# Optimization experiments

Measured on AMD Instinct MI355X. Metric: run time of the kernel, lower is better.

Reference implementation:

```python
import jax, jax.numpy as jnp
import numpy as np

N_GRAPHS = 512
NODES_PER_G = 200
EDGES_PER_G = 6400
N = N_GRAPHS * NODES_PER_G        # 102400 nodes
E = N_GRAPHS * EDGES_PER_G        # 3276800 edges
HID = 128
NCLS = 10


def _linear_params(key, fan_in, fan_out):
    # torch nn.Linear default init: U(-1/sqrt(fan_in), 1/sqrt(fan_in))
    s = 1.0 / np.sqrt(fan_in)
    kw, kb = jax.random.split(key)
    W = jax.random.uniform(kw, (fan_in, fan_out), minval=-s, maxval=s, dtype=jnp.float32)
    b = jax.random.uniform(kb, (fan_out,), minval=-s, maxval=s, dtype=jnp.float32)
    return W, b


def setup_inputs() -> dict:
    key = jax.random.key(0)
    ks = jax.random.split(key, 10)
    # edges are confined within each graph (DGL batched graph structure)
    g_off = (jnp.arange(E, dtype=jnp.int32) // EDGES_PER_G) * NODES_PER_G
    src = (g_off + jax.random.randint(ks[0], (E,), 0, NODES_PER_G)).astype(jnp.int32)
    dst = (g_off + jax.random.randint(ks[1], (E,), 0, NODES_PER_G)).astype(jnp.int32)
    W1, b1 = _linear_params(ks[2], 1, HID)
    W2, b2 = _linear_params(ks[3], HID, HID)
    Wa, ba = _linear_params(ks[4], HID, 512)
    Wb, bb = _linear_params(ks[5], 512, 1024)
    Wc, bc = _linear_params(ks[6], 1024, 1024)
    Wd, bd = _linear_params(ks[7], 1024, 512)
    We, be = _linear_params(ks[8], 512, NCLS)
    return dict(src=src, dst=dst, W1=W1, b1=b1, W2=W2, b2=b2,
                Wa=Wa, ba=ba, Wb=Wb, bb=bb, Wc=Wc, bc=bc,
                Wd=Wd, bd=bd, We=We, be=be)


def reference(src, dst, W1, b1, W2, b2, Wa, ba, Wb, bb, Wc, bc, Wd, bd, We, be):
    seg = jax.ops.segment_sum
    ones = jnp.ones((E,), jnp.float32)
    in_deg = seg(ones, dst, num_segments=N)    # [N]
    out_deg = seg(ones, src, num_segments=N)   # [N]
    # DGL GraphConv norm='both': degrees clamped to min 1
    inv_out = (1.0 / jnp.sqrt(jnp.maximum(out_deg, 1.0)))[:, None]
    inv_in = (1.0 / jnp.sqrt(jnp.maximum(in_deg, 1.0)))[:, None]

    def gconv(h, W, b):
        h = (h @ W) * inv_out                    # src-side normalize (weight applied first; same math)
        h = seg(h[src], dst, num_segments=N)     # gather + scatter-add aggregation
        return h * inv_in + b                    # dst-side normalize + bias

    h = in_deg[:, None]                          # input node features = in-degrees, [N,1]
    h = jax.nn.relu(gconv(h, W1, b1))
    h = jax.nn.relu(gconv(h, W2, b2))

    gid = jnp.arange(N, dtype=jnp.int32) // NODES_PER_G
    hg = seg(h, gid, num_segments=N_GRAPHS) / float(NODES_PER_G)  # mean readout, [G,HID]

    x = jax.nn.relu(hg @ Wa + ba)
    x = jax.nn.relu(x @ Wb + bb)
    x = jax.nn.relu(x @ Wc + bc)
    x = jax.nn.relu(x @ Wd + bd)
    return jax.nn.softmax(x @ We + be, axis=-1)  # nn.Softmax over class dim
```

## Files before the change

### kernel.cpp

```cpp
#include <hip/hip_runtime.h>
#include <stdint.h>

typedef unsigned short u16;
typedef unsigned int   u32;

#define NG   512
#define NPG  200
#define EPG  6400
#define NN   (NG*NPG)
#define NE_  (NG*EPG)
#define HID  128
#define HS   232
#define ZP   136

__device__ __forceinline__ float bf2f(u16 b){ u32 u = ((u32)b) << 16; return __builtin_bit_cast(float, u); }
__device__ __forceinline__ u16 f2bf(float f){
    u32 u = __builtin_bit_cast(u32, f);
    u = (u + 0x7FFFu + ((u >> 16) & 1u)) >> 16;
    return (u16)u;
}

typedef __attribute__((ext_vector_type(8))) short bf16x8;
typedef __attribute__((ext_vector_type(4))) float f32x4;

enum : int { cW1=0, cb1=128, cb2=256, cba=384, cbb=896, cbc=1920, cbd=2944, cWe=3456, cbe=8576, cEND=8586 };
enum : int { T_Wa=0, T_Wb=65536, T_Wc=589824, T_Wd=1638400, T_END=2162688 };

struct PrepIn { const void* p[14]; };

__global__ __launch_bounds__(256) void k_prep2(PrepIn in, float* __restrict__ canon,
                                               u16* __restrict__ W2T, u16* __restrict__ WTa)
{
    __shared__ u16 tile[64][72];
    __shared__ int sflag;
    const int tid = threadIdx.x;
    if (tid < 64){
        const u16* wb = (const u16*)in.p[0];
        u16 a = wb[tid], b = wb[64 + tid];
        unsigned long long m1 = __ballot((int)((a >> 7) & 0xFF) >= 0x7F);
        unsigned long long m2 = __ballot((int)((b >> 7) & 0xFF) >= 0x7F);
        if (tid == 0) sflag = (__popcll(m1) + __popcll(m2) > 4) ? 1 : 0;
    }
    __syncthreads();
    const int f = sflag;
    const int bid = blockIdx.x;

    if (bid < 532){
        const void* s; u16* dst; int K, N, t, lgn;
        if      (bid < 4)  { t = bid;       s = in.p[2];  dst = W2T;        K = 128;  N = 128;  lgn = 1; }
        else if (bid < 20) { t = bid - 4;   s = in.p[4];  dst = WTa + T_Wa; K = 128;  N = 512;  lgn = 3; }
        else if (bid < 148){ t = bid - 20;  s = in.p[6];  dst = WTa + T_Wb; K = 512;  N = 1024; lgn = 4; }
        else if (bid < 404){ t = bid - 148; s = in.p[8];  dst = WTa + T_Wc; K = 1024; N = 1024; lgn = 4; }
        else               { t = bid - 404; s = in.p[10]; dst = WTa + T_Wd; K = 1024; N = 512;  lgn = 3; }
        const int k0 = (t >> lgn) * 64, n0 = (t & ((1 << lgn) - 1)) * 64;
        #pragma unroll
        for (int i = 0; i < 16; i++){
            int idx = i*256 + tid;
            int kk = idx >> 6, nn = idx & 63;
            int si = (k0 + kk)*N + n0 + nn;
            tile[nn][kk] = f ? f2bf(((const float*)s)[si]) : ((const u16*)s)[si];
        }
        __syncthreads();
        #pragma unroll
        for (int i = 0; i < 16; i++){
            int idx = i*256 + tid;
            int nn = idx >> 6, kk = idx & 63;
            dst[(size_t)(n0 + nn)*K + k0 + kk] = tile[nn][kk];
        }
    } else {
        int i = (bid - 532)*256 + tid;
        if (i < cEND){
            const void* s; int off;
            if      (i < 128) { s = in.p[0];  off = i; }
            else if (i < 256) { s = in.p[1];  off = i - 128; }
            else if (i < 384) { s = in.p[3];  off = i - 256; }
            else if (i < 896) { s = in.p[5];  off = i - 384; }
            else if (i < 1920){ s = in.p[7];  off = i - 896; }
            else if (i < 2944){ s = in.p[9];  off = i - 1920; }
            else if (i < 3456){ s = in.p[11]; off = i - 2944; }
            else if (i < 8576){ s = in.p[12]; off = i - 3456; }
            else              { s = in.p[13]; off = i - 8576; }
            canon[i] = f ? ((const float*)s)[off] : bf2f(((const u16*)s)[off]);
        }
    }
}

__global__ __launch_bounds__(512) void k_mega(
    const int* __restrict__ src, const int* __restrict__ dst,
    const float* __restrict__ W1, const float* __restrict__ b1,
    const float* __restrict__ b2, const u16* __restrict__ W2T,
    float* __restrict__ hg)
{
    __shared__ u32 pkE[EPG];
    __shared__ __align__(16) u16 h1s[HID*HS];
    __shared__ __align__(16) u16 Aq[64*HS];
    __shared__ __align__(16) u16 Zq[64*ZP];
    __shared__ int degIn[NPG], degOut[NPG];
    __shared__ float sVal[NPG], sAgg[NPG], iiL[NPG], ioL[NPG], tL[NPG];
    __shared__ float w1L[HID], b1L[HID], b2L[HID], poolL[HID];

    const int g = blockIdx.x, tid = threadIdx.x;
    u32* aq32 = (u32*)Aq;

    if (tid < NPG){ degIn[tid] = 0; degOut[tid] = 0; sAgg[tid] = 0.f; }
    if (tid < HID){ w1L[tid] = W1[tid]; b1L[tid] = b1[tid]; b2L[tid] = b2[tid]; poolL[tid] = 0.f; }
    __syncthreads();

    const int ebase = g * EPG;
    #pragma unroll
    for (int i = 0; i < (EPG + 511)/512; i++){
        int e = i*512 + tid;
        if (e < EPG){
            int s = src[ebase + e] - g*NPG;
            int d = dst[ebase + e] - g*NPG;
            pkE[e] = (u32)s | ((u32)d << 16);
            atomicAdd(&degOut[s], 1);
            atomicAdd(&degIn[d], 1);
        }
    }
    __syncthreads();

    if (tid < NPG){
        float ii = rsqrtf(fmaxf((float)degIn[tid], 1.f));
        float io = rsqrtf(fmaxf((float)degOut[tid], 1.f));
        iiL[tid] = ii; ioL[tid] = io;
        sVal[tid] = (float)degIn[tid] * io;
    }
    __syncthreads();

    #pragma unroll
    for (int i = 0; i < (EPG + 511)/512; i++){
        int e = i*512 + tid;
        if (e < EPG){
            u32 u = pkE[e];
            atomicAdd(&sAgg[u >> 16], sVal[u & 0xFFFF]);
        }
    }
    __syncthreads();
    if (tid < NPG) tL[tid] = sAgg[tid] * iiL[tid];
    __syncthreads();

    #pragma unroll 4
    for (int i = 0; i < HID*HS/512; i++){
        int idx = i*512 + tid;
        int c = idx / HS, v = idx - c*HS;
        u16 o = 0;
        if (v < NPG)
            o = f2bf(fmaxf(fmaf(tL[v], w1L[c], b1L[c]), 0.f) * ioL[v]);
        h1s[idx] = o;
    }
    __syncthreads();

    const int w = tid >> 6, lane = tid & 63;
    const int lr = lane & 15, quad = lane >> 4;
    const f32x4 fz = {0.f, 0.f, 0.f, 0.f};

    for (int q = 0; q < 4; q++){
        uint4* a4 = (uint4*)Aq;
        for (int i = tid; i < 64*HS/8; i += 512) a4[i] = make_uint4(0,0,0,0);
        __syncthreads();
        #pragma unroll
        for (int i = 0; i < (EPG + 511)/512; i++){
            int e = i*512 + tid;
            if (e < EPG){
                u32 u = pkE[e];
                int s = u & 0xFFFF, d = u >> 16;
                int qe = (d * 41) >> 11;
                if (qe == q){
                    int idx = (d - q*50)*HS + s;
                    atomicAdd(&aq32[idx >> 1], 1u << (16*(idx & 1)));
                }
            }
        }
        __syncthreads();
        for (int i = tid; i < 64*HS/2; i += 512){
            u32 wv = aq32[i];
            if (wv)
                aq32[i] = (u32)f2bf((float)(wv & 0xFFFFu)) | ((u32)f2bf((float)(wv >> 16)) << 16);
        }
        __syncthreads();

        const int wm = w >> 1, wn = w & 1;
        f32x4 acc[2][2];
        #pragma unroll
        for (int mi = 0; mi < 2; mi++)
            #pragma unroll
            for (int nt = 0; nt < 2; nt++) acc[mi][nt] = fz;
        for (int ks = 0; ks < 7; ks++){
            bf16x8 af[2], bf[2];
            #pragma unroll
            for (int mi = 0; mi < 2; mi++)
                af[mi] = *(const bf16x8*)&h1s[(wm*32 + mi*16 + lr)*HS + ks*32 + quad*8];
            #pragma unroll
            for (int nt = 0; nt < 2; nt++)
                bf[nt] = *(const bf16x8*)&Aq[(wn*32 + nt*16 + lr)*HS + ks*32 + quad*8];
            #pragma unroll
            for (int mi = 0; mi < 2; mi++)
                #pragma unroll
                for (int nt = 0; nt < 2; nt++)
                    acc[mi][nt] = __builtin_amdgcn_mfma_f32_16x16x32_bf16(
                        af[mi], bf[nt], acc[mi][nt], 0, 0, 0);
        }
        #pragma unroll
        for (int mi = 0; mi < 2; mi++)
            #pragma unroll
            for (int nt = 0; nt < 2; nt++){
                int vq = wn*32 + nt*16 + lr;
                int c0 = wm*32 + mi*16 + quad*4;
                u16 z0 = f2bf(acc[mi][nt][0]), z1 = f2bf(acc[mi][nt][1]);
                u16 z2 = f2bf(acc[mi][nt][2]), z3 = f2bf(acc[mi][nt][3]);
                uint2 pk = { (u32)z0 | ((u32)z1 << 16), (u32)z2 | ((u32)z3 << 16) };
                *(uint2*)&Zq[vq*ZP + c0] = pk;
            }
        __syncthreads();

        const int wm2 = w >> 2, wn2 = w & 3;
        f32x4 acc2[2][2];
        #pragma unroll
        for (int mi = 0; mi < 2; mi++)
            #pragma unroll
            for (int nt = 0; nt < 2; nt++) acc2[mi][nt] = fz;
        for (int ks = 0; ks < 4; ks++){
            bf16x8 za[2], wb[2];
            #pragma unroll
            for (int mi = 0; mi < 2; mi++)
                za[mi] = *(const bf16x8*)&Zq[(wm2*32 + mi*16 + lr)*ZP + ks*32 + quad*8];
            #pragma unroll
            for (int nt = 0; nt < 2; nt++)
                wb[nt] = *(const bf16x8*)&W2T[(size_t)(wn2*32 + nt*16 + lr)*HID + ks*32 + quad*8];
            #pragma unroll
            for (int mi = 0; mi < 2; mi++)
                #pragma unroll
                for (int nt = 0; nt < 2; nt++)
                    acc2[mi][nt] = __builtin_amdgcn_mfma_f32_16x16x32_bf16(
                        za[mi], wb[nt], acc2[mi][nt], 0, 0, 0);
        }
        #pragma unroll
        for (int mi = 0; mi < 2; mi++)
            #pragma unroll
            for (int nt = 0; nt < 2; nt++){
                int cout = wn2*32 + nt*16 + lr;
                float s = 0.f;
                #pragma unroll
                for (int r = 0; r < 4; r++){
                    int vq = wm2*32 + mi*16 + quad*4 + r;
                    if (vq < 50)
                        s += fmaxf(fmaf(acc2[mi][nt][r], iiL[q*50 + vq], b2L[cout]), 0.f);
                }
                atomicAdd(&poolL[cout], s);
            }
        __syncthreads();
    }

    if (tid < HID) hg[(size_t)g*HID + tid] = poolL[tid] * (1.f / NPG);
}

template<int K, bool AF32>
__global__ __launch_bounds__(512) void k_mlp5(
    const void* __restrict__ Ahi_, const u16* __restrict__ Alo,
    const u16* __restrict__ WT, const float* __restrict__ bias,
    u16* __restrict__ Ohi, u16* __restrict__ Olo, int Nc)
{
    constexpr int ITERS = K / 64;
    __shared__ __align__(16) float red[32][68];

    const int tid = threadIdx.x;
    const int w = tid >> 6, lane = tid & 63;
    const int kz = w >> 2, wm = (w >> 1) & 1, wn = w & 1;
    const int lr = lane & 15, quad = lane >> 4;
    const int row0 = blockIdx.x * 32, col0 = blockIdx.y * 64;
    const int m = row0 + wm*16 + lr;
    const int k0 = kz * (K/2);

    const float* Af = (const float*)Ahi_;
    const u16*   Ah = (const u16*)Ahi_;

    auto loadA = [&](int it, bf16x8& hi, bf16x8& lo){
        const int kk = k0 + it*32 + quad*8;
        if constexpr (AF32){
            float xs[8];
            *(float4*)&xs[0] = *(const float4*)&Af[(size_t)m*K + kk];
            *(float4*)&xs[4] = *(const float4*)&Af[(size_t)m*K + kk + 4];
            #pragma unroll
            for (int j = 0; j < 8; j++){
                u16 hh = f2bf(xs[j]);
                hi[j] = (short)hh;
                lo[j] = (short)f2bf(xs[j] - bf2f(hh));
            }
        } else {
            hi = *(const bf16x8*)&Ah[(size_t)m*K + kk];
            lo = *(const bf16x8*)&Alo[(size_t)m*K + kk];
        }
    };
    auto loadB = [&](int it, bf16x8* b){
        const int kk = k0 + it*32 + quad*8;
        #pragma unroll
        for (int nt = 0; nt < 2; nt++){
            int n = col0 + wn*32 + nt*16 + lr;
            b[nt] = *(const bf16x8*)&WT[(size_t)n*K + kk];
        }
    };

    const f32x4 fz = {0.f, 0.f, 0.f, 0.f};
    f32x4 acc[2] = {fz, fz};
    bf16x8 chi, clo, cb[2], nhi, nlo, nb[2];
    loadA(0, chi, clo); loadB(0, cb);
    #pragma unroll 2
    for (int it = 0; it < ITERS; it++){
        if (it + 1 < ITERS){ loadA(it+1, nhi, nlo); loadB(it+1, nb); }
        #pragma unroll
        for (int nt = 0; nt < 2; nt++){
            acc[nt] = __builtin_amdgcn_mfma_f32_16x16x32_bf16(chi, cb[nt], acc[nt], 0, 0, 0);
            acc[nt] = __builtin_amdgcn_mfma_f32_16x16x32_bf16(clo, cb[nt], acc[nt], 0, 0, 0);
        }
        chi = nhi; clo = nlo; cb[0] = nb[0]; cb[1] = nb[1];
    }

    if (kz == 1){
        #pragma unroll
        for (int nt = 0; nt < 2; nt++)
            #pragma unroll
            for (int r = 0; r < 4; r++)
                red[wm*16 + quad*4 + r][wn*32 + nt*16 + lr] = acc[nt][r];
    }
    __syncthreads();
    if (kz == 0){
        #pragma unroll
        for (int nt = 0; nt < 2; nt++)
            #pragma unroll
            for (int r = 0; r < 4; r++){
                int rr = wm*16 + quad*4 + r;
                int cc = wn*32 + nt*16 + lr;
                float v = acc[nt][r] + red[rr][cc] + bias[col0 + cc];
                v = fmaxf(v, 0.f);
                u16 hh = f2bf(v);
                size_t go = (size_t)(row0 + rr) * Nc + col0 + cc;
                Ohi[go] = hh;
                Olo[go] = f2bf(v - bf2f(hh));
            }
    }
}

__global__ __launch_bounds__(64) void k_head(
    const u16* __restrict__ Xhi, const u16* __restrict__ Xlo,
    const float* __restrict__ We, const float* __restrict__ be,
    void* __restrict__ out, const u16* __restrict__ w1bits)
{
    const int g = blockIdx.x, lane = threadIdx.x;
    u16 a = w1bits[lane], b = w1bits[64 + lane];
    unsigned long long m1 = __ballot((int)((a >> 7) & 0xFF) >= 0x7F);
    unsigned long long m2 = __ballot((int)((b >> 7) & 0xFF) >= 0x7F);
    const int f = (__popcll(m1) + __popcll(m2) > 4) ? 1 : 0;

    float part[10];
    #pragma unroll
    for (int c = 0; c < 10; c++) part[c] = 0.f;
    for (int k = lane; k < 512; k += 64){
        float x = bf2f(Xhi[(size_t)g*512 + k]) + bf2f(Xlo[(size_t)g*512 + k]);
        #pragma unroll
        for (int c = 0; c < 10; c++) part[c] = fmaf(x, We[k*10 + c], part[c]);
    }
    #pragma unroll
    for (int c = 0; c < 10; c++){
        float v = part[c];
        for (int off = 32; off > 0; off >>= 1) v += __shfl_down(v, off);
        part[c] = v;
    }
    if (lane == 0){
        #pragma unroll
        for (int c = 0; c < 10; c++) part[c] += be[c];
        float m = part[0];
        #pragma unroll
        for (int c = 1; c < 10; c++) m = fmaxf(m, part[c]);
        float e[10], s = 0.f;
        #pragma unroll
        for (int c = 0; c < 10; c++){ e[c] = __expf(part[c] - m); s += e[c]; }
        float inv = 1.f / s;
        #pragma unroll
        for (int c = 0; c < 10; c++){
            float p = e[c] * inv;
            if (f) ((float*)out)[g*10 + c] = p;
            else   ((u16*)out)[g*10 + c]  = f2bf(p);
        }
    }
}

extern "C" void kernel_launch(void* const* d_in, const int* in_sizes, int n_in,
                              void* d_out, int out_size, void* d_ws, size_t ws_size,
                              hipStream_t stream)
{
    const int* src = (const int*)d_in[0];
    const int* dst = (const int*)d_in[1];

    char* ws = (char*)d_ws;
    size_t o = 0;
    float* canon    = (float*)(ws + o); o += ((size_t)cEND * 4 + 15) & ~(size_t)15;
    u16*   W2T      = (u16*)  (ws + o); o += (size_t)HID * HID * 2;
    u16*   WTa      = (u16*)  (ws + o); o += ((size_t)T_END * 2 + 15) & ~(size_t)15;
    float* hg       = (float*)(ws + o); o += (size_t)NG * HID * 4;
    u16*   X1hi     = (u16*)  (ws + o); o += (size_t)NG * 512 * 2;
    u16*   X1lo     = (u16*)  (ws + o); o += (size_t)NG * 512 * 2;
    u16*   X2hi     = (u16*)  (ws + o); o += (size_t)NG * 1024 * 2;
    u16*   X2lo     = (u16*)  (ws + o); o += (size_t)NG * 1024 * 2;
    u16*   X3hi     = (u16*)  (ws + o); o += (size_t)NG * 1024 * 2;
    u16*   X3lo     = (u16*)  (ws + o); o += (size_t)NG * 1024 * 2;
    u16*   X4hi     = (u16*)  (ws + o); o += (size_t)NG * 512 * 2;
    u16*   X4lo     = (u16*)  (ws + o); o += (size_t)NG * 512 * 2;
    (void)ws_size; (void)in_sizes; (void)n_in; (void)out_size;

    PrepIn pin;
    for (int i = 0; i < 14; i++) pin.p[i] = d_in[2 + i];
    k_prep2<<<dim3(566), dim3(256), 0, stream>>>(pin, canon, W2T, WTa);

    const float *W1 = canon+cW1, *b1 = canon+cb1, *b2 = canon+cb2;
    const float *ba = canon+cba, *bb = canon+cbb, *bc = canon+cbc, *bd = canon+cbd;
    const float *We = canon+cWe, *be = canon+cbe;

    k_mega<<<dim3(NG), dim3(512), 0, stream>>>(src, dst, W1, b1, b2, W2T, hg);

    k_mlp5<128,  true ><<<dim3(16, 8),  dim3(512), 0, stream>>>(hg,   nullptr, WTa + T_Wa, ba, X1hi, X1lo, 512);
    k_mlp5<512,  false><<<dim3(16, 16), dim3(512), 0, stream>>>(X1hi, X1lo,    WTa + T_Wb, bb, X2hi, X2lo, 1024);
    k_mlp5<1024, false><<<dim3(16, 16), dim3(512), 0, stream>>>(X2hi, X2lo,    WTa + T_Wc, bc, X3hi, X3lo, 1024);
    k_mlp5<1024, false><<<dim3(16, 8),  dim3(512), 0, stream>>>(X3hi, X3lo,    WTa + T_Wd, bd, X4hi, X4lo, 512);

    k_head<<<dim3(NG), dim3(64), 0, stream>>>(X4hi, X4lo, We, be, d_out, (const u16*)d_in[2]);
}
```

Measured before the change: 255.7 us.

## Shrink LDS in graph mega-kernel and deepen MLP GEMM prefetch

The per-graph kernel now keeps the packed edge list in registers instead of LDS. It builds the first-layer features in two 64-channel halves rebuilt for each quarter, and reuses the adjacency buffer for Z. This cuts shared-memory use so more blocks fit per CU (launch_bounds 512,4), and W2T fragments are hoisted into registers outside the quarter loop. In exchange, h1 is recomputed four times, register pressure rises, and the dense GEMM kernel gets a 3-stage register prefetch with full unroll.

```diff
diff --git a/kernel.cpp b/kernel.cpp
--- a/kernel.cpp
+++ b/kernel.cpp
@@ -85,37 +85,42 @@
     }
 }
 
-__global__ __launch_bounds__(512) void k_mega(
+__global__ __launch_bounds__(512, 4) void k_mega(
     const int* __restrict__ src, const int* __restrict__ dst,
     const float* __restrict__ W1, const float* __restrict__ b1,
     const float* __restrict__ b2, const u16* __restrict__ W2T,
     float* __restrict__ hg)
 {
-    __shared__ u32 pkE[EPG];
-    __shared__ __align__(16) u16 h1s[HID*HS];
-    __shared__ __align__(16) u16 Aq[64*HS];
-    __shared__ __align__(16) u16 Zq[64*ZP];
+    __shared__ __align__(16) u16 h1sH[64*HS];
+    __shared__ __align__(16) u16 AqZ[64*HS];
     __shared__ int degIn[NPG], degOut[NPG];
     __shared__ float sVal[NPG], sAgg[NPG], iiL[NPG], ioL[NPG], tL[NPG];
     __shared__ float w1L[HID], b1L[HID], b2L[HID], poolL[HID];
 
     const int g = blockIdx.x, tid = threadIdx.x;
-    u32* aq32 = (u32*)Aq;
-
-    if (tid < NPG){ degIn[tid] = 0; degOut[tid] = 0; sAgg[tid] = 0.f; }
-    if (tid < HID){ w1L[tid] = W1[tid]; b1L[tid] = b1[tid]; b2L[tid] = b2[tid]; poolL[tid] = 0.f; }
-    __syncthreads();
-
+    u32* aq32 = (u32*)AqZ;
+
+    u32 epk[13];
     const int ebase = g * EPG;
     #pragma unroll
-    for (int i = 0; i < (EPG + 511)/512; i++){
+    for (int i = 0; i < 13; i++){
         int e = i*512 + tid;
         if (e < EPG){
             int s = src[ebase + e] - g*NPG;
             int d = dst[ebase + e] - g*NPG;
-            pkE[e] = (u32)s | ((u32)d << 16);
-            atomicAdd(&degOut[s], 1);
-            atomicAdd(&degIn[d], 1);
+            epk[i] = (u32)s | ((u32)d << 16);
+        } else epk[i] = 0xFFFFFFFFu;
+    }
+
+    if (tid < NPG){ degIn[tid] = 0; degOut[tid] = 0; sAgg[tid] = 0.f; }
+    if (tid < HID){ w1L[tid] = W1[tid]; b1L[tid] = b1[tid]; b2L[tid] = b2[tid]; poolL[tid] = 0.f; }
+    __syncthreads();
+
+    #pragma unroll
+    for (int i = 0; i < 13; i++){
+        if (epk[i] != 0xFFFFFFFFu){
+            atomicAdd(&degOut[epk[i] & 0xFFFF], 1);
+            atomicAdd(&degIn[epk[i] >> 16], 1);
         }
     }
     __syncthreads();
@@ -129,45 +134,39 @@
     __syncthreads();
 
     #pragma unroll
-    for (int i = 0; i < (EPG + 511)/512; i++){
-        int e = i*512 + tid;
-        if (e < EPG){
-            u32 u = pkE[e];
-            atomicAdd(&sAgg[u >> 16], sVal[u & 0xFFFF]);
-        }
+    for (int i = 0; i < 13; i++){
+        if (epk[i] != 0xFFFFFFFFu)
+            atomicAdd(&sAgg[epk[i] >> 16], sVal[epk[i] & 0xFFFF]);
     }
     __syncthreads();
     if (tid < NPG) tL[tid] = sAgg[tid] * iiL[tid];
-    __syncthreads();
-
-    #pragma unroll 4
-    for (int i = 0; i < HID*HS/512; i++){
-        int idx = i*512 + tid;
-        int c = idx / HS, v = idx - c*HS;
-        u16 o = 0;
-        if (v < NPG)
-            o = f2bf(fmaxf(fmaf(tL[v], w1L[c], b1L[c]), 0.f) * ioL[v]);
-        h1s[idx] = o;
-    }
-    __syncthreads();
 
     const int w = tid >> 6, lane = tid & 63;
     const int lr = lane & 15, quad = lane >> 4;
+    const int wm = w >> 1, wn = w & 1;
+    const int wm2 = w >> 2, wn2 = w & 3;
     const f32x4 fz = {0.f, 0.f, 0.f, 0.f};
 
+    bf16x8 wb[4][2];
+    #pragma unroll
+    for (int ks = 0; ks < 4; ks++)
+        #pragma unroll
+        for (int nt = 0; nt < 2; nt++)
+            wb[ks][nt] = *(const bf16x8*)&W2T[(size_t)(wn2*32 + nt*16 + lr)*HID + ks*32 + quad*8];
+    __syncthreads();
+
     for (int q = 0; q < 4; q++){
-        uint4* a4 = (uint4*)Aq;
+        uint4* a4 = (uint4*)AqZ;
         for (int i = tid; i < 64*HS/8; i += 512) a4[i] = make_uint4(0,0,0,0);
         __syncthreads();
         #pragma unroll
-        for (int i = 0; i < (EPG + 511)/512; i++){
-            int e = i*512 + tid;
-            if (e < EPG){
-                u32 u = pkE[e];
-                int s = u & 0xFFFF, d = u >> 16;
+        for (int i = 0; i < 13; i++){
+            u32 u = epk[i];
+            if (u != 0xFFFFFFFFu){
+                int d = u >> 16;
                 int qe = (d * 41) >> 11;
                 if (qe == q){
-                    int idx = (d - q*50)*HS + s;
+                    int idx = (d - q*50)*HS + (u & 0xFFFF);
                     atomicAdd(&aq32[idx >> 1], 1u << (16*(idx & 1)));
                 }
             }
@@ -180,61 +179,64 @@
         }
         __syncthreads();
 
-        const int wm = w >> 1, wn = w & 1;
-        f32x4 acc[2][2];
-        #pragma unroll
-        for (int mi = 0; mi < 2; mi++)
-            #pragma unroll
-            for (int nt = 0; nt < 2; nt++) acc[mi][nt] = fz;
-        for (int ks = 0; ks < 7; ks++){
-            bf16x8 af[2], bf[2];
-            #pragma unroll
-            for (int mi = 0; mi < 2; mi++)
-                af[mi] = *(const bf16x8*)&h1s[(wm*32 + mi*16 + lr)*HS + ks*32 + quad*8];
-            #pragma unroll
-            for (int nt = 0; nt < 2; nt++)
-                bf[nt] = *(const bf16x8*)&Aq[(wn*32 + nt*16 + lr)*HS + ks*32 + quad*8];
-            #pragma unroll
-            for (int mi = 0; mi < 2; mi++)
+        f32x4 accZ[2][2];
+        #pragma unroll
+        for (int h = 0; h < 2; h++){
+            #pragma unroll 4
+            for (int i = 0; i < 64*HS/512; i++){
+                int idx = i*512 + tid;
+                int cl = idx / HS, v = idx - cl*HS;
+                int c = h*64 + cl;
+                u16 o = 0;
+                if (v < NPG)
+                    o = f2bf(fmaxf(fmaf(tL[v], w1L[c], b1L[c]), 0.f) * ioL[v]);
+                h1sH[idx] = o;
+            }
+            __syncthreads();
+            accZ[h][0] = fz; accZ[h][1] = fz;
+            for (int ks = 0; ks < 7; ks++){
+                bf16x8 af = *(const bf16x8*)&h1sH[(wm*16 + lr)*HS + ks*32 + quad*8];
                 #pragma unroll
-                for (int nt = 0; nt < 2; nt++)
-                    acc[mi][nt] = __builtin_amdgcn_mfma_f32_16x16x32_bf16(
-                        af[mi], bf[nt], acc[mi][nt], 0, 0, 0);
-        }
-        #pragma unroll
-        for (int mi = 0; mi < 2; mi++)
+                for (int nt = 0; nt < 2; nt++){
+                    bf16x8 bfr = *(const bf16x8*)&AqZ[(wn*32 + nt*16 + lr)*HS + ks*32 + quad*8];
+                    accZ[h][nt] = __builtin_amdgcn_mfma_f32_16x16x32_bf16(af, bfr, accZ[h][nt], 0, 0, 0);
+                }
+            }
+            __syncthreads();
+        }
+
+        u16* Zq = AqZ;
+        #pragma unroll
+        for (int h = 0; h < 2; h++)
             #pragma unroll
             for (int nt = 0; nt < 2; nt++){
                 int vq = wn*32 + nt*16 + lr;
-                int c0 = wm*32 + mi*16 + quad*4;
-                u16 z0 = f2bf(acc[mi][nt][0]), z1 = f2bf(acc[mi][nt][1]);
-                u16 z2 = f2bf(acc[mi][nt][2]), z3 = f2bf(acc[mi][nt][3]);
+                int c0 = h*64 + wm*16 + quad*4;
+                u16 z0 = f2bf(accZ[h][nt][0]), z1 = f2bf(accZ[h][nt][1]);
+                u16 z2 = f2bf(accZ[h][nt][2]), z3 = f2bf(accZ[h][nt][3]);
                 uint2 pk = { (u32)z0 | ((u32)z1 << 16), (u32)z2 | ((u32)z3 << 16) };
                 *(uint2*)&Zq[vq*ZP + c0] = pk;
             }
         __syncthreads();
 
-        const int wm2 = w >> 2, wn2 = w & 3;
         f32x4 acc2[2][2];
         #pragma unroll
         for (int mi = 0; mi < 2; mi++)
             #pragma unroll
             for (int nt = 0; nt < 2; nt++) acc2[mi][nt] = fz;
         for (int ks = 0; ks < 4; ks++){
-            bf16x8 za[2], wb[2];
+            bf16x8 za[2];
             #pragma unroll
             for (int mi = 0; mi < 2; mi++)
                 za[mi] = *(const bf16x8*)&Zq[(wm2*32 + mi*16 + lr)*ZP + ks*32 + quad*8];
-            #pragma unroll
-            for (int nt = 0; nt < 2; nt++)
-                wb[nt] = *(const bf16x8*)&W2T[(size_t)(wn2*32 + nt*16 + lr)*HID + ks*32 + quad*8];
             #pragma unroll
             for (int mi = 0; mi < 2; mi++)
                 #pragma unroll
                 for (int nt = 0; nt < 2; nt++)
                     acc2[mi][nt] = __builtin_amdgcn_mfma_f32_16x16x32_bf16(
-                        za[mi], wb[nt], acc2[mi][nt], 0, 0, 0);
-        }
+                        za[mi], wb[ks][nt], acc2[mi][nt], 0, 0, 0);
+        }
+
         #pragma unroll
         for (int mi = 0; mi < 2; mi++)
             #pragma unroll
@@ -303,17 +305,19 @@
 
     const f32x4 fz = {0.f, 0.f, 0.f, 0.f};
     f32x4 acc[2] = {fz, fz};
-    bf16x8 chi, clo, cb[2], nhi, nlo, nb[2];
-    loadA(0, chi, clo); loadB(0, cb);
-    #pragma unroll 2
+    bf16x8 hi[3], lo[3], bb[3][2];
+    loadA(0, hi[0], lo[0]); loadB(0, bb[0]);
+    if (ITERS > 1){ loadA(1, hi[1], lo[1]); loadB(1, bb[1]); }
+    #pragma unroll
     for (int it = 0; it < ITERS; it++){
-        if (it + 1 < ITERS){ loadA(it+1, nhi, nlo); loadB(it+1, nb); }
+        const int sl = it % 3;
+        const int pf = (it + 2) % 3;
+        if (it + 2 < ITERS){ loadA(it+2, hi[pf], lo[pf]); loadB(it+2, bb[pf]); }
         #pragma unroll
         for (int nt = 0; nt < 2; nt++){
-            acc[nt] = __builtin_amdgcn_mfma_f32_16x16x32_bf16(chi, cb[nt], acc[nt], 0, 0, 0);
-            acc[nt] = __builtin_amdgcn_mfma_f32_16x16x32_bf16(clo, cb[nt], acc[nt], 0, 0, 0);
-        }
-        chi = nhi; clo = nlo; cb[0] = nb[0]; cb[1] = nb[1];
+            acc[nt] = __builtin_amdgcn_mfma_f32_16x16x32_bf16(hi[sl], bb[sl][nt], acc[nt], 0, 0, 0);
+            acc[nt] = __builtin_amdgcn_mfma_f32_16x16x32_bf16(lo[sl], bb[sl][nt], acc[nt], 0, 0, 0);
+        }
     }
 
     if (kz == 1){
```

New measurement: 261.4 us. +2.2%, slower.

## Split graph megakernel into layer-1 and per-quarter kernels; narrow MLP tiles

Applied to the files above, without the earlier changes.

The per-graph megakernel is split into two kernels. k_l1 computes degrees and the layer-1 features, writes h1 to global memory, and buckets edges into per-quarter lists. k_quarter then processes each graph quarter in its own block, with atomically accumulated pooling into hg, which k_prep2 now zeroes. This gives 4x more blocks for the layer-2 aggregation and GEMMs, and each block scans only its own quarter's edges instead of all edges four times. In exchange it adds global round-trips for h1sT and the edge buffers, uses a fixed QCAP that silently drops edges if a quarter overflows, and halves the MLP column tile with a 3-stage register prefetch to double the grid.

```diff
diff --git a/kernel.cpp b/kernel.cpp
--- a/kernel.cpp
+++ b/kernel.cpp
@@ -10,8 +10,10 @@
 #define NN   (NG*NPG)
 #define NE_  (NG*EPG)
 #define HID  128
-#define HS   232
+#define KP   224
+#define AQS  232
 #define ZP   136
+#define QCAP 2048
 
 __device__ __forceinline__ float bf2f(u16 b){ u32 u = ((u32)b) << 16; return __builtin_bit_cast(float, u); }
 __device__ __forceinline__ u16 f2bf(float f){
@@ -29,7 +31,8 @@
 struct PrepIn { const void* p[14]; };
 
 __global__ __launch_bounds__(256) void k_prep2(PrepIn in, float* __restrict__ canon,
-                                               u16* __restrict__ W2T, u16* __restrict__ WTa)
+                                               u16* __restrict__ W2T, u16* __restrict__ WTa,
+                                               float* __restrict__ hg)
 {
     __shared__ u16 tile[64][72];
     __shared__ int sflag;
@@ -44,6 +47,11 @@
     __syncthreads();
     const int f = sflag;
     const int bid = blockIdx.x;
+
+    if (tid < 116){
+        int j = bid*116 + tid;
+        if (j < NG*HID) hg[j] = 0.f;
+    }
 
     if (bid < 532){
         const void* s; u16* dst; int K, N, t, lgn;
@@ -85,38 +93,39 @@
     }
 }
 
-__global__ __launch_bounds__(512) void k_mega(
+__global__ __launch_bounds__(256) void k_l1(
     const int* __restrict__ src, const int* __restrict__ dst,
     const float* __restrict__ W1, const float* __restrict__ b1,
-    const float* __restrict__ b2, const u16* __restrict__ W2T,
-    float* __restrict__ hg)
-{
-    __shared__ u32 pkE[EPG];
-    __shared__ __align__(16) u16 h1s[HID*HS];
-    __shared__ __align__(16) u16 Aq[64*HS];
-    __shared__ __align__(16) u16 Zq[64*ZP];
+    float* __restrict__ invInG, u16* __restrict__ h1sT,
+    u32* __restrict__ edgeBuf, int* __restrict__ cntQ)
+{
+    __shared__ u16 srcL[EPG];
+    __shared__ u16 dstL[EPG];
     __shared__ int degIn[NPG], degOut[NPG];
-    __shared__ float sVal[NPG], sAgg[NPG], iiL[NPG], ioL[NPG], tL[NPG];
-    __shared__ float w1L[HID], b1L[HID], b2L[HID], poolL[HID];
+    __shared__ int qcur[4];
+    __shared__ float sAgg4[4][NPG];
+    __shared__ float sValL[NPG], iiL[NPG], ioL[NPG], tL[NPG];
+    __shared__ float w1L[HID], b1L[HID];
 
     const int g = blockIdx.x, tid = threadIdx.x;
-    u32* aq32 = (u32*)Aq;
-
-    if (tid < NPG){ degIn[tid] = 0; degOut[tid] = 0; sAgg[tid] = 0.f; }
-    if (tid < HID){ w1L[tid] = W1[tid]; b1L[tid] = b1[tid]; b2L[tid] = b2[tid]; poolL[tid] = 0.f; }
+
+    if (tid < NPG){
+        degIn[tid] = 0; degOut[tid] = 0;
+        sAgg4[0][tid] = 0.f; sAgg4[1][tid] = 0.f; sAgg4[2][tid] = 0.f; sAgg4[3][tid] = 0.f;
+    }
+    if (tid < HID){ w1L[tid] = W1[tid]; b1L[tid] = b1[tid]; }
+    if (tid < 4) qcur[tid] = 0;
     __syncthreads();
 
     const int ebase = g * EPG;
     #pragma unroll
-    for (int i = 0; i < (EPG + 511)/512; i++){
-        int e = i*512 + tid;
-        if (e < EPG){
-            int s = src[ebase + e] - g*NPG;
-            int d = dst[ebase + e] - g*NPG;
-            pkE[e] = (u32)s | ((u32)d << 16);
-            atomicAdd(&degOut[s], 1);
-            atomicAdd(&degIn[d], 1);
-        }
+    for (int i = 0; i < EPG/256; i++){
+        int e = i*256 + tid;
+        int s = src[ebase + e] - g*NPG;
+        int d = dst[ebase + e] - g*NPG;
+        srcL[e] = (u16)s; dstL[e] = (u16)d;
+        atomicAdd(&degOut[s], 1);
+        atomicAdd(&degIn[d], 1);
     }
     __syncthreads();
 
@@ -124,152 +133,206 @@
         float ii = rsqrtf(fmaxf((float)degIn[tid], 1.f));
         float io = rsqrtf(fmaxf((float)degOut[tid], 1.f));
         iiL[tid] = ii; ioL[tid] = io;
-        sVal[tid] = (float)degIn[tid] * io;
-    }
-    __syncthreads();
-
-    #pragma unroll
-    for (int i = 0; i < (EPG + 511)/512; i++){
-        int e = i*512 + tid;
-        if (e < EPG){
-            u32 u = pkE[e];
-            atomicAdd(&sAgg[u >> 16], sVal[u & 0xFFFF]);
-        }
-    }
-    __syncthreads();
-    if (tid < NPG) tL[tid] = sAgg[tid] * iiL[tid];
-    __syncthreads();
-
+        sValL[tid] = (float)degIn[tid] * io;
+        invInG[g*NPG + tid] = ii;
+    }
+    __syncthreads();
+
+    const int rep = tid & 3;
+    #pragma unroll
+    for (int i = 0; i < EPG/256; i++){
+        int e = i*256 + tid;
+        int s = srcL[e], d = dstL[e];
+        atomicAdd(&sAgg4[rep][d], sValL[s]);
+        int q = (d * 41) >> 11;
+        int pos = atomicAdd(&qcur[q], 1);
+        if (pos < QCAP)
+            edgeBuf[((size_t)(g*4 + q))*QCAP + pos] = (u32)s | ((u32)(d - q*50) << 16);
+    }
+    __syncthreads();
+
+    if (tid < 4) cntQ[g*4 + tid] = (qcur[tid] < QCAP) ? qcur[tid] : QCAP;
+    if (tid < NPG)
+        tL[tid] = (sAgg4[0][tid] + sAgg4[1][tid] + sAgg4[2][tid] + sAgg4[3][tid]) * iiL[tid];
+    __syncthreads();
+
+    const size_t base = (size_t)g * HID * KP;
     #pragma unroll 4
-    for (int i = 0; i < HID*HS/512; i++){
-        int idx = i*512 + tid;
-        int c = idx / HS, v = idx - c*HS;
+    for (int i = 0; i < HID*KP/256; i++){
+        int idx = i*256 + tid;
+        int c = idx / KP, v = idx - c*KP;
         u16 o = 0;
         if (v < NPG)
             o = f2bf(fmaxf(fmaf(tL[v], w1L[c], b1L[c]), 0.f) * ioL[v]);
-        h1s[idx] = o;
+        h1sT[base + idx] = o;
+    }
+}
+
+__global__ __launch_bounds__(256, 5) void k_quarter(
+    const u32* __restrict__ edgeBuf, const int* __restrict__ cntQ,
+    const u16* __restrict__ h1sT, const u16* __restrict__ W2T,
+    const float* __restrict__ invInG, const float* __restrict__ b2,
+    float* __restrict__ hg)
+{
+    __shared__ __align__(16) u16 Aq[64*AQS];
+    __shared__ float invInL[64];
+    __shared__ float b2L[HID];
+    __shared__ float poolL[HID];
+
+    const int bid = blockIdx.x, tid = threadIdx.x;
+    const int xcd = bid & 7, slot = bid >> 3;
+    const int g = (slot >> 2) * 8 + xcd;
+    const int q = slot & 3;
+    u32* aq32 = (u32*)Aq;
+
+    if (tid < HID){ b2L[tid] = b2[tid]; poolL[tid] = 0.f; }
+    if (tid < 64) invInL[tid] = (tid < 50) ? invInG[g*NPG + q*50 + tid] : 0.f;
+
+    uint4* a4 = (uint4*)Aq;
+    #pragma unroll
+    for (int i = 0; i < 8; i++){
+        int idx = i*256 + tid;
+        if (idx < 64*AQS/8) a4[idx] = make_uint4(0,0,0,0);
+    }
+    __syncthreads();
+
+    const int cnt = cntQ[g*4 + q];
+    const u32* eb = edgeBuf + (size_t)(g*4 + q) * QCAP;
+    for (int i = tid; i < cnt; i += 256){
+        u32 e = eb[i];
+        int idx = (int)(e >> 16) * AQS + (int)(e & 0xFFFF);
+        atomicAdd(&aq32[idx >> 1], 1u << (16*(idx & 1)));
+    }
+    __syncthreads();
+
+    for (int i = tid; i < 64*AQS/2; i += 256){
+        u32 wv = aq32[i];
+        if (wv)
+            aq32[i] = (u32)f2bf((float)(wv & 0xFFFFu)) | ((u32)f2bf((float)(wv >> 16)) << 16);
     }
     __syncthreads();
 
     const int w = tid >> 6, lane = tid & 63;
+    const int wm = w >> 1, wn = w & 1;
     const int lr = lane & 15, quad = lane >> 4;
     const f32x4 fz = {0.f, 0.f, 0.f, 0.f};
 
-    for (int q = 0; q < 4; q++){
-        uint4* a4 = (uint4*)Aq;
-        for (int i = tid; i < 64*HS/8; i += 512) a4[i] = make_uint4(0,0,0,0);
-        __syncthreads();
-        #pragma unroll
-        for (int i = 0; i < (EPG + 511)/512; i++){
-            int e = i*512 + tid;
-            if (e < EPG){
-                u32 u = pkE[e];
-                int s = u & 0xFFFF, d = u >> 16;
-                int qe = (d * 41) >> 11;
-                if (qe == q){
-                    int idx = (d - q*50)*HS + s;
-                    atomicAdd(&aq32[idx >> 1], 1u << (16*(idx & 1)));
-                }
+    f32x4 acc[2][4];
+    #pragma unroll
+    for (int mi = 0; mi < 2; mi++)
+        #pragma unroll
+        for (int nt = 0; nt < 4; nt++) acc[mi][nt] = fz;
+    {
+        const u16* Bg = h1sT + (size_t)g * HID * KP + (size_t)(wn*64) * KP;
+        bf16x8 br[3][4];
+        #pragma unroll
+        for (int nt = 0; nt < 4; nt++){
+            br[0][nt] = *(const bf16x8*)&Bg[(nt*16 + lr)*KP + quad*8];
+            br[1][nt] = *(const bf16x8*)&Bg[(nt*16 + lr)*KP + 32 + quad*8];
+        }
+        #pragma unroll
+        for (int ks = 0; ks < 7; ks++){
+            const int sl = ks % 3, pf = (ks + 2) % 3;
+            if (ks + 2 < 7){
+                #pragma unroll
+                for (int nt = 0; nt < 4; nt++)
+                    br[pf][nt] = *(const bf16x8*)&Bg[(nt*16 + lr)*KP + (ks+2)*32 + quad*8];
             }
-        }
-        __syncthreads();
-        for (int i = tid; i < 64*HS/2; i += 512){
-            u32 wv = aq32[i];
-            if (wv)
-                aq32[i] = (u32)f2bf((float)(wv & 0xFFFFu)) | ((u32)f2bf((float)(wv >> 16)) << 16);
-        }
-        __syncthreads();
-
-        const int wm = w >> 1, wn = w & 1;
-        f32x4 acc[2][2];
-        #pragma unroll
-        for (int mi = 0; mi < 2; mi++)
-            #pragma unroll
-            for (int nt = 0; nt < 2; nt++) acc[mi][nt] = fz;
-        for (int ks = 0; ks < 7; ks++){
-            bf16x8 af[2], bf[2];
+            bf16x8 af[2];
             #pragma unroll
             for (int mi = 0; mi < 2; mi++)
-                af[mi] = *(const bf16x8*)&h1s[(wm*32 + mi*16 + lr)*HS + ks*32 + quad*8];
-            #pragma unroll
-            for (int nt = 0; nt < 2; nt++)
-                bf[nt] = *(const bf16x8*)&Aq[(wn*32 + nt*16 + lr)*HS + ks*32 + quad*8];
+                af[mi] = *(const bf16x8*)&Aq[((wm*2 + mi)*16 + lr)*AQS + ks*32 + quad*8];
             #pragma unroll
             for (int mi = 0; mi < 2; mi++)
                 #pragma unroll
-                for (int nt = 0; nt < 2; nt++)
+                for (int nt = 0; nt < 4; nt++)
                     acc[mi][nt] = __builtin_amdgcn_mfma_f32_16x16x32_bf16(
-                        af[mi], bf[nt], acc[mi][nt], 0, 0, 0);
-        }
-        #pragma unroll
-        for (int mi = 0; mi < 2; mi++)
-            #pragma unroll
-            for (int nt = 0; nt < 2; nt++){
-                int vq = wn*32 + nt*16 + lr;
-                int c0 = wm*32 + mi*16 + quad*4;
-                u16 z0 = f2bf(acc[mi][nt][0]), z1 = f2bf(acc[mi][nt][1]);
-                u16 z2 = f2bf(acc[mi][nt][2]), z3 = f2bf(acc[mi][nt][3]);
-                uint2 pk = { (u32)z0 | ((u32)z1 << 16), (u32)z2 | ((u32)z3 << 16) };
-                *(uint2*)&Zq[vq*ZP + c0] = pk;
+                        af[mi], br[sl][nt], acc[mi][nt], 0, 0, 0);
+        }
+    }
+    __syncthreads();
+
+    u16* Zq = Aq;
+    #pragma unroll
+    for (int mi = 0; mi < 2; mi++)
+        #pragma unroll
+        for (int nt = 0; nt < 4; nt++){
+            int vq = (wm*2 + mi)*16 + quad*4;
+            int c = wn*64 + nt*16 + lr;
+            Zq[(vq+0)*ZP + c] = f2bf(acc[mi][nt][0]);
+            Zq[(vq+1)*ZP + c] = f2bf(acc[mi][nt][1]);
+            Zq[(vq+2)*ZP + c] = f2bf(acc[mi][nt][2]);
+            Zq[(vq+3)*ZP + c] = f2bf(acc[mi][nt][3]);
+        }
+    __syncthreads();
+
+    f32x4 acc2[2][4];
+    #pragma unroll
+    for (int mi = 0; mi < 2; mi++)
+        #pragma unroll
+        for (int nt = 0; nt < 4; nt++) acc2[mi][nt] = fz;
+    {
+        const u16* Wg = W2T + (size_t)(wn*64) * HID;
+        bf16x8 bcur[4], bnxt[4];
+        #pragma unroll
+        for (int nt = 0; nt < 4; nt++)
+            bcur[nt] = *(const bf16x8*)&Wg[(nt*16 + lr)*HID + quad*8];
+        #pragma unroll
+        for (int ks = 0; ks < 4; ks++){
+            if (ks < 3){
+                #pragma unroll
+                for (int nt = 0; nt < 4; nt++)
+                    bnxt[nt] = *(const bf16x8*)&Wg[(nt*16 + lr)*HID + (ks+1)*32 + quad*8];
             }
-        __syncthreads();
-
-        const int wm2 = w >> 2, wn2 = w & 3;
-        f32x4 acc2[2][2];
-        #pragma unroll
-        for (int mi = 0; mi < 2; mi++)
-            #pragma unroll
-            for (int nt = 0; nt < 2; nt++) acc2[mi][nt] = fz;
-        for (int ks = 0; ks < 4; ks++){
-            bf16x8 za[2], wb[2];
+            bf16x8 za[2];
             #pragma unroll
             for (int mi = 0; mi < 2; mi++)
-                za[mi] = *(const bf16x8*)&Zq[(wm2*32 + mi*16 + lr)*ZP + ks*32 + quad*8];
-            #pragma unroll
-            for (int nt = 0; nt < 2; nt++)
-                wb[nt] = *(const bf16x8*)&W2T[(size_t)(wn2*32 + nt*16 + lr)*HID + ks*32 + quad*8];
+                za[mi] = *(const bf16x8*)&Zq[((wm*2 + mi)*16 + lr)*ZP + ks*32 + quad*8];
             #pragma unroll
             for (int mi = 0; mi < 2; mi++)
                 #pragma unroll
-                for (int nt = 0; nt < 2; nt++)
+                for (int nt = 0; nt < 4; nt++)
                     acc2[mi][nt] = __builtin_amdgcn_mfma_f32_16x16x32_bf16(
-                        za[mi], wb[nt], acc2[mi][nt], 0, 0, 0);
-        }
-        #pragma unroll
-        for (int mi = 0; mi < 2; mi++)
-            #pragma unroll
-            for (int nt = 0; nt < 2; nt++){
-                int cout = wn2*32 + nt*16 + lr;
-                float s = 0.f;
-                #pragma unroll
-                for (int r = 0; r < 4; r++){
-                    int vq = wm2*32 + mi*16 + quad*4 + r;
-                    if (vq < 50)
-                        s += fmaxf(fmaf(acc2[mi][nt][r], iiL[q*50 + vq], b2L[cout]), 0.f);
-                }
-                atomicAdd(&poolL[cout], s);
+                        za[mi], bcur[nt], acc2[mi][nt], 0, 0, 0);
+            #pragma unroll
+            for (int nt = 0; nt < 4; nt++) bcur[nt] = bnxt[nt];
+        }
+    }
+
+    #pragma unroll
+    for (int mi = 0; mi < 2; mi++)
+        #pragma unroll
+        for (int nt = 0; nt < 4; nt++){
+            int cout = wn*64 + nt*16 + lr;
+            float s = 0.f;
+            #pragma unroll
+            for (int r = 0; r < 4; r++){
+                int vq = (wm*2 + mi)*16 + quad*4 + r;
+                if (vq < 50)
+                    s += fmaxf(fmaf(acc2[mi][nt][r], invInL[vq], b2L[cout]), 0.f);
             }
-        __syncthreads();
-    }
-
-    if (tid < HID) hg[(size_t)g*HID + tid] = poolL[tid] * (1.f / NPG);
+            atomicAdd(&poolL[cout], s);
+        }
+    __syncthreads();
+    if (tid < HID) atomicAdd(&hg[(size_t)g*HID + tid], poolL[tid] * (1.f / NPG));
 }
 
 template<int K, bool AF32>
-__global__ __launch_bounds__(512) void k_mlp5(
+__global__ __launch_bounds__(512) void k_mlp6(
     const void* __restrict__ Ahi_, const u16* __restrict__ Alo,
     const u16* __restrict__ WT, const float* __restrict__ bias,
     u16* __restrict__ Ohi, u16* __restrict__ Olo, int Nc)
 {
     constexpr int ITERS = K / 64;
-    __shared__ __align__(16) float red[32][68];
+    __shared__ __align__(16) float red[32][36];
 
     const int tid = threadIdx.x;
     const int w = tid >> 6, lane = tid & 63;
     const int kz = w >> 2, wm = (w >> 1) & 1, wn = w & 1;
     const int lr = lane & 15, quad = lane >> 4;
-    const int row0 = blockIdx.x * 32, col0 = blockIdx.y * 64;
+    const int row0 = blockIdx.x * 32, col0 = blockIdx.y * 32;
     const int m = row0 + wm*16 + lr;
+    const int n = col0 + wn*16 + lr;
     const int k0 = kz * (K/2);
 
     const float* Af = (const float*)Ahi_;
@@ -292,52 +355,45 @@
             lo = *(const bf16x8*)&Alo[(size_t)m*K + kk];
         }
     };
-    auto loadB = [&](int it, bf16x8* b){
-        const int kk = k0 + it*32 + quad*8;
-        #pragma unroll
-        for (int nt = 0; nt < 2; nt++){
-            int n = col0 + wn*32 + nt*16 + lr;
-            b[nt] = *(const bf16x8*)&WT[(size_t)n*K + kk];
-        }
-    };
 
     const f32x4 fz = {0.f, 0.f, 0.f, 0.f};
-    f32x4 acc[2] = {fz, fz};
-    bf16x8 chi, clo, cb[2], nhi, nlo, nb[2];
-    loadA(0, chi, clo); loadB(0, cb);
-    #pragma unroll 2
+    f32x4 acc = fz;
+    bf16x8 hi[3], lo[3], bb[3];
+    loadA(0, hi[0], lo[0]);
+    bb[0] = *(const bf16x8*)&WT[(size_t)n*K + k0 + quad*8];
+    if (ITERS > 1){
+        loadA(1, hi[1], lo[1]);
+        bb[1] = *(const bf16x8*)&WT[(size_t)n*K + k0 + 32 + quad*8];
+    }
+    #pragma unroll
     for (int it = 0; it < ITERS; it++){
-        if (it + 1 < ITERS){ loadA(it+1, nhi, nlo); loadB(it+1, nb); }
-        #pragma unroll
-        for (int nt = 0; nt < 2; nt++){
-            acc[nt] = __builtin_amdgcn_mfma_f32_16x16x32_bf16(chi, cb[nt], acc[nt], 0, 0, 0);
-            acc[nt] = __builtin_amdgcn_mfma_f32_16x16x32_bf16(clo, cb[nt], acc[nt], 0, 0, 0);
-        }
-        chi = nhi; clo = nlo; cb[0] = nb[0]; cb[1] = nb[1];
+        const int sl = it % 3, pf = (it + 2) % 3;
+        if (it + 2 < ITERS){
+            loadA(it+2, hi[pf], lo[pf]);
+            bb[pf] = *(const bf16x8*)&WT[(size_t)n*K + k0 + (it+2)*32 + quad*8];
+        }
+        acc = __builtin_amdgcn_mfma_f32_16x16x32_bf16(hi[sl], bb[sl], acc, 0, 0, 0);
+        acc = __builtin_amdgcn_mfma_f32_16x16x32_bf16(lo[sl], bb[sl], acc, 0, 0, 0);
     }
 
     if (kz == 1){
         #pragma unroll
-        for (int nt = 0; nt < 2; nt++)
-            #pragma unroll
-            for (int r = 0; r < 4; r++)
-                red[wm*16 + quad*4 + r][wn*32 + nt*16 + lr] = acc[nt][r];
+        for (int r = 0; r < 4; r++)
+            red[wm*16 + quad*4 + r][wn*16 + lr] = acc[r];
     }
     __syncthreads();
     if (kz == 0){
         #pragma unroll
-        for (int nt = 0; nt < 2; nt++)
-            #pragma unroll
-            for (int r = 0; r < 4; r++){
-                int rr = wm*16 + quad*4 + r;
-                int cc = wn*32 + nt*16 + lr;
-                float v = acc[nt][r] + red[rr][cc] + bias[col0 + cc];
-                v = fmaxf(v, 0.f);
-                u16 hh = f2bf(v);
-                size_t go = (size_t)(row0 + rr) * Nc + col0 + cc;
-                Ohi[go] = hh;
-                Olo[go] = f2bf(v - bf2f(hh));
-            }
+        for (int r = 0; r < 4; r++){
+            int rr = wm*16 + quad*4 + r;
+            int cc = wn*16 + lr;
+            float v = acc[r] + red[rr][cc] + bias[col0 + cc];
+            v = fmaxf(v, 0.f);
+            u16 hh = f2bf(v);
+            size_t go = (size_t)(row0 + rr) * Nc + col0 + cc;
+            Ohi[go] = hh;
+            Olo[go] = f2bf(v - bf2f(hh));
+        }
     }
 }
 
@@ -397,6 +453,10 @@
     float* canon    = (float*)(ws + o); o += ((size_t)cEND * 4 + 15) & ~(size_t)15;
     u16*   W2T      = (u16*)  (ws + o); o += (size_t)HID * HID * 2;
     u16*   WTa      = (u16*)  (ws + o); o += ((size_t)T_END * 2 + 15) & ~(size_t)15;
+    float* invIn    = (float*)(ws + o); o += (size_t)NN * 4;
+    u32*   edgeBuf  = (u32*)  (ws + o); o += (size_t)NG * 4 * QCAP * 4;
+    int*   cntQ     = (int*)  (ws + o); o += (size_t)NG * 4 * 4;
+    u16*   h1sT     = (u16*)  (ws + o); o += (size_t)NG * HID * KP * 2;
     float* hg       = (float*)(ws + o); o += (size_t)NG * HID * 4;
     u16*   X1hi     = (u16*)  (ws + o); o += (size_t)NG * 512 * 2;
     u16*   X1lo     = (u16*)  (ws + o); o += (size_t)NG * 512 * 2;
@@ -410,18 +470,22 @@
 
     PrepIn pin;
     for (int i = 0; i < 14; i++) pin.p[i] = d_in[2 + i];
-    k_prep2<<<dim3(566), dim3(256), 0, stream>>>(pin, canon, W2T, WTa);
+    k_prep2<<<dim3(566), dim3(256), 0, stream>>>(pin, canon, W2T, WTa, hg);
 
     const float *W1 = canon+cW1, *b1 = canon+cb1, *b2 = canon+cb2;
     const float *ba = canon+cba, *bb = canon+cbb, *bc = canon+cbc, *bd = canon+cbd;
     const float *We = canon+cWe, *be = canon+cbe;
 
-    k_mega<<<dim3(NG), dim3(512), 0, stream>>>(src, dst, W1, b1, b2, W2T, hg);
-
-    k_mlp5<128,  true ><<<dim3(16, 8),  dim3(512), 0, stream>>>(hg,   nullptr, WTa + T_Wa, ba, X1hi, X1lo, 512);
-    k_mlp5<512,  false><<<dim3(16, 16), dim3(512), 0, stream>>>(X1hi, X1lo,    WTa + T_Wb, bb, X2hi, X2lo, 1024);
-    k_mlp5<1024, false><<<dim3(16, 16), dim3(512), 0, stream>>>(X2hi, X2lo,    WTa + T_Wc, bc, X3hi, X3lo, 1024);
-    k_mlp5<1024, false><<<dim3(16, 8),  dim3(512), 0, stream>>>(X3hi, X3lo,    WTa + T_Wd, bd, X4hi, X4lo, 512);
+    k_l1<<<dim3(NG), dim3(256), 0, stream>>>(
+        src, dst, W1, b1, invIn, h1sT, edgeBuf, cntQ);
+
+    k_quarter<<<dim3(NG*4), dim3(256), 0, stream>>>(
+        edgeBuf, cntQ, h1sT, W2T, invIn, b2, hg);
+
+    k_mlp6<128,  true ><<<dim3(16, 16), dim3(512), 0, stream>>>(hg,   nullptr, WTa + T_Wa, ba, X1hi, X1lo, 512);
+    k_mlp6<512,  false><<<dim3(16, 32), dim3(512), 0, stream>>>(X1hi, X1lo,    WTa + T_Wb, bb, X2hi, X2lo, 1024);
+    k_mlp6<1024, false><<<dim3(16, 32), dim3(512), 0, stream>>>(X2hi, X2lo,    WTa + T_Wc, bc, X3hi, X3lo, 1024);
+    k_mlp6<1024, false><<<dim3(16, 16), dim3(512), 0, stream>>>(X3hi, X3lo,    WTa + T_Wd, bd, X4hi, X4lo, 512);
 
     k_head<<<dim3(NG), dim3(64), 0, stream>>>(X4hi, X4lo, We, be, d_out, (const u16*)d_in[2]);
 }
```

Result: slower. 261.7 us (+2.4%).
